# Performance work log

Measured on AMD Instinct MI355X. Metric: run time of the kernel, lower is better.

Reference implementation:

```python
import jax, jax.numpy as jnp
import numpy as np

N = 262144        # 64^3 grid unknowns
NNZ = 7 * N       # ~7-point stencil sparsity
BS = 32


def setup_inputs() -> dict:
    key = jax.random.key(0)
    k1, k2, k3, k4, k5 = jax.random.split(key, 5)
    y_pred = jax.random.normal(k1, (BS, N), dtype=jnp.float32)
    y_true = jax.random.normal(k2, (BS, N), dtype=jnp.float32)
    A_vals = jax.random.normal(k3, (NNZ,), dtype=jnp.float32)
    A_rows = jax.random.randint(k4, (NNZ,), 0, N, dtype=jnp.int32)
    A_cols = jax.random.randint(k5, (NNZ,), 0, N, dtype=jnp.int32)
    return {"y_pred": y_pred, "y_true": y_true, "A_vals": A_vals,
            "A_rows": A_rows, "A_cols": A_cols}


def reference(y_pred, y_true, A_vals, A_rows, A_cols):
    # YhatY[b] = <y_true[b], y_pred[b]>
    YhatY = jnp.sum(y_true * y_pred, axis=1)                      # (bs,)
    # Sparse matvec per batch: YhatAt = (A @ y_pred.T).T, COO form.
    # gathered[e, b] = A_vals[e] * y_pred[b, A_cols[e]]
    gathered = (y_pred[:, A_cols] * A_vals).T                     # (nnz, bs)
    YhatAt = jax.ops.segment_sum(gathered, A_rows, num_segments=N).T  # (bs, N)
    # YhatYhatAt[b] = <y_pred[b], A y_pred[b]>
    YhatYhatAt = jnp.sum(y_pred * YhatAt, axis=1)                 # (bs,)
    # diag(YhatY / YhatYhatAt) @ YhatAt == row-wise scale by alpha
    alpha = YhatY / YhatYhatAt                                    # (bs,)
    resid = y_true - alpha[:, None] * YhatAt                      # (bs, N)
    return jnp.mean(jnp.sum(resid * resid, axis=1))
```

## Files before the change

### kernel.cpp

```cpp
#include <hip/hip_runtime.h>

#define NGRID 262144
#define NNZ_C 1835008
#define TP    260


__global__ __launch_bounds__(256) void k_prep(
        const float* __restrict__ yp, const float* __restrict__ yt,
        float* __restrict__ yp_t, float* __restrict__ yat_t,
        float* __restrict__ p1) {
    __shared__ __align__(16) float T[32 * TP];
    __shared__ float p1red[32];
    const int tid = threadIdx.x;
    const int l = tid & 63, w = tid >> 6;
    const size_t n0 = (size_t)blockIdx.x * 256;
    #pragma unroll
    for (int s = 0; s < 8; ++s) {
        const int b = s * 4 + w;
        const float4 a = *(const float4*)(yp + (size_t)b * NGRID + n0 + 4 * l);
        const float4 t = *(const float4*)(yt + (size_t)b * NGRID + n0 + 4 * l);
        *(float4*)(&T[b * TP + 4 * l]) = a;
        float sty = a.x * t.x + a.y * t.y + a.z * t.z + a.w * t.w;
        #pragma unroll
        for (int o = 32; o > 0; o >>= 1) sty += __shfl_down(sty, o);
        if (l == 0) p1red[b] = sty;
    }
    __syncthreads();
    float4* ypt4 = (float4*)(yp_t + n0 * 32);
    float4* yat4 = (float4*)(yat_t + n0 * 32);
    #pragma unroll
    for (int q = 0; q < 8; ++q) {
        const int f = q * 256 + tid;
        const int n = f >> 3;
        const int bb = 4 * (f & 7);
        float4 v;
        v.x = T[(bb + 0) * TP + n];
        v.y = T[(bb + 1) * TP + n];
        v.z = T[(bb + 2) * TP + n];
        v.w = T[(bb + 3) * TP + n];
        ypt4[f] = v;
        yat4[f] = make_float4(0.f, 0.f, 0.f, 0.f);
    }
    if (tid < 32) p1[blockIdx.x * 32 + tid] = p1red[tid];
}

__global__ void k_scatter(const float* __restrict__ vals,
                          const int* __restrict__ rows,
                          const int* __restrict__ cols,
                          const float* __restrict__ yp_t,
                          float* __restrict__ yat_t) {
    const size_t tid = (size_t)blockIdx.x * blockDim.x + threadIdx.x;
    const int b = (int)(tid & 31);
    const size_t e = tid >> 5;
    const float v = vals[e];
    const int r = rows[e];
    const int c = cols[e];
    const float x = yp_t[(size_t)c * 32 + b];
    atomicAdd(&yat_t[(size_t)r * 32 + b], v * x);
}

__global__ __launch_bounds__(256) void k_post(
        const float* __restrict__ yat_t, const float* __restrict__ yp_t,
        const float* __restrict__ yt, float* __restrict__ p2) {
    __shared__ float tile[256 * 33];
    __shared__ float red[2][256];
    const int tid = threadIdx.x;
    const size_t n0 = (size_t)blockIdx.x * 256;

    float c1 = 0.f, c3 = 0.f;
    #pragma unroll
    for (int i = 0; i < 32; ++i) {
        const int f = i * 256 + tid;
        const float a = yat_t[n0 * 32 + f];
        const float p = yp_t[n0 * 32 + f];
        c1 = fmaf(p, a, c1);
        c3 = fmaf(a, a, c3);
        tile[(f >> 5) * 33 + (f & 31)] = a;
    }
    red[0][tid] = c1;
    red[1][tid] = c3;
    __syncthreads();

    const int w = tid >> 6;
    const int lane = tid & 63;
    #pragma unroll
    for (int j = 0; j < 8; ++j) {
        const int b = w * 8 + j;
        const float* ytr = yt + (size_t)b * NGRID + n0;
        float c2 = 0.f, tt = 0.f;
        #pragma unroll
        for (int c = 0; c < 4; ++c) {
            const int nl = c * 64 + lane;
            const float t = ytr[nl];
            const float yv = tile[nl * 33 + b];
            c2 = fmaf(t, yv, c2);
            tt = fmaf(t, t, tt);
        }
        #pragma unroll
        for (int o = 32; o > 0; o >>= 1) {
            c2 += __shfl_down(c2, o);
            tt += __shfl_down(tt, o);
        }
        if (lane == 0) {
            p2[blockIdx.x * 128 + 32 + b] = c2;
            p2[blockIdx.x * 128 + 96 + b] = tt;
        }
    }

    if (tid < 32) {
        float s1 = 0.f, s3 = 0.f;
        #pragma unroll
        for (int k = 0; k < 8; ++k) {
            s1 += red[0][tid + 32 * k];
            s3 += red[1][tid + 32 * k];
        }
        p2[blockIdx.x * 128 + 0 + tid] = s1;
        p2[blockIdx.x * 128 + 64 + tid] = s3;
    }
}

__global__ __launch_bounds__(256) void k_finish(
        const float* __restrict__ p2, const float* __restrict__ p1,
        float* __restrict__ out) {
    __shared__ float tot[128];
    __shared__ float styv[32];
    __shared__ float lb[32];
    const int tid = threadIdx.x;
    if (tid < 128) {
        float acc = 0.f;
        for (int j = 0; j < 1024; ++j) acc += p2[(size_t)j * 128 + tid];
        tot[tid] = acc;
    } else if (tid < 160) {
        const int b = tid - 128;
        float acc = 0.f;
        for (int j = 0; j < 1024; ++j) acc += p1[(size_t)j * 32 + b];
        styv[b] = acc;
    }
    __syncthreads();
    if (tid < 32) {
        const float c1 = tot[tid];
        const float c2 = tot[32 + tid];
        const float c3 = tot[64 + tid];
        const float stt = tot[96 + tid];
        const float a = styv[tid] / c1;
        lb[tid] = fmaf(a * a, c3, fmaf(-2.f * a, c2, stt));
    }
    __syncthreads();
    if (tid == 0) {
        float s = 0.f;
        #pragma unroll
        for (int i = 0; i < 32; ++i) s += lb[i];
        out[0] = s * (1.0f / 32.0f);
    }
}

extern "C" void kernel_launch(void* const* d_in, const int* in_sizes, int n_in,
                              void* d_out, int out_size, void* d_ws, size_t ws_size,
                              hipStream_t stream) {
    const float* yp = (const float*)d_in[0];
    const float* yt = (const float*)d_in[1];
    const float* Av = (const float*)d_in[2];
    const int*   Ar = (const int*)d_in[3];
    const int*   Ac = (const int*)d_in[4];
    float* out = (float*)d_out;

    float* ws    = (float*)d_ws;
    float* yp_t  = ws;
    float* yat_t = yp_t + (size_t)NGRID * 32;
    float* p1    = yat_t + (size_t)NGRID * 32;
    float* p2    = p1 + 1024 * 32;

    k_prep<<<NGRID / 256, 256, 0, stream>>>(yp, yt, yp_t, yat_t, p1);
    k_scatter<<<(NNZ_C * 32) / 256, 256, 0, stream>>>(Av, Ar, Ac, yp_t, yat_t);
    k_post<<<NGRID / 256, 256, 0, stream>>>(yat_t, yp_t, yt, p2);
    k_finish<<<1, 256, 0, stream>>>(p2, p1, out);
}
```

Measured before the change: 348.1 us.

## Use packed float2 atomics in scatter, vectorize post loads, split final reduction

The scatter kernel now handles two batch columns per thread and issues packed v2f32 atomic adds where the builtin exists, halving the atomic instruction count and thread count. k_post reads y_true with float4 loads and gathers its per-batch sums through shared memory. The single-block final reduction over 1024 partials becomes a two-stage reduction across 64 blocks plus one block. Packed atomics depend on compiler builtin availability, and if neither is present the code falls back to two scalar atomics.

```diff
diff --git a/kernel.cpp b/kernel.cpp
--- a/kernel.cpp
+++ b/kernel.cpp
@@ -4,6 +4,15 @@
 #define NNZ_C 1835008
 #define TP    260
 
+
+typedef float v2f __attribute__((ext_vector_type(2)));
+#ifdef __has_builtin
+#if __has_builtin(__builtin_amdgcn_flat_atomic_fadd_v2f32)
+#define PK_FADD_FLAT 1
+#elif __has_builtin(__builtin_amdgcn_global_atomic_fadd_v2f32)
+#define PK_FADD_GLOBAL 1
+#endif
+#endif
 
 __global__ __launch_bounds__(256) void k_prep(
         const float* __restrict__ yp, const float* __restrict__ yt,
@@ -50,13 +59,24 @@
                           const float* __restrict__ yp_t,
                           float* __restrict__ yat_t) {
     const size_t tid = (size_t)blockIdx.x * blockDim.x + threadIdx.x;
-    const int b = (int)(tid & 31);
-    const size_t e = tid >> 5;
+    const int b2 = (int)(tid & 15);
+    const size_t e = tid >> 4;
     const float v = vals[e];
     const int r = rows[e];
     const int c = cols[e];
-    const float x = yp_t[(size_t)c * 32 + b];
-    atomicAdd(&yat_t[(size_t)r * 32 + b], v * x);
+    const float2 x = *(const float2*)(yp_t + (size_t)c * 32 + 2 * b2);
+    float* dst = yat_t + (size_t)r * 32 + 2 * b2;
+#if defined(PK_FADD_FLAT)
+    v2f add; add.x = v * x.x; add.y = v * x.y;
+    __builtin_amdgcn_flat_atomic_fadd_v2f32((v2f*)dst, add);
+#elif defined(PK_FADD_GLOBAL)
+    v2f add; add.x = v * x.x; add.y = v * x.y;
+    __builtin_amdgcn_global_atomic_fadd_v2f32(
+        (__attribute__((address_space(1))) v2f*)(unsigned long long)dst, add);
+#else
+    atomicAdd(dst, v * x.x);
+    atomicAdd(dst + 1, v * x.y);
+#endif
 }
 
 __global__ __launch_bounds__(256) void k_post(
@@ -64,7 +84,9 @@
         const float* __restrict__ yt, float* __restrict__ p2) {
     __shared__ float tile[256 * 33];
     __shared__ float red[2][256];
+    __shared__ float c2red[32], ttred[32];
     const int tid = threadIdx.x;
+    const int l = tid & 63, w = tid >> 6;
     const size_t n0 = (size_t)blockIdx.x * 256;
 
     float c1 = 0.f, c3 = 0.f;
@@ -81,31 +103,22 @@
     red[1][tid] = c3;
     __syncthreads();
 
-    const int w = tid >> 6;
-    const int lane = tid & 63;
-    #pragma unroll
-    for (int j = 0; j < 8; ++j) {
-        const int b = w * 8 + j;
-        const float* ytr = yt + (size_t)b * NGRID + n0;
-        float c2 = 0.f, tt = 0.f;
-        #pragma unroll
-        for (int c = 0; c < 4; ++c) {
-            const int nl = c * 64 + lane;
-            const float t = ytr[nl];
-            const float yv = tile[nl * 33 + b];
-            c2 = fmaf(t, yv, c2);
-            tt = fmaf(t, t, tt);
-        }
+    #pragma unroll
+    for (int s = 0; s < 8; ++s) {
+        const int b = 4 * s + w;
+        const float4 t = *(const float4*)(yt + (size_t)b * NGRID + n0 + 4 * l);
+        const int n = 4 * l;
+        float c2 = t.x * tile[(n + 0) * 33 + b] + t.y * tile[(n + 1) * 33 + b]
+                 + t.z * tile[(n + 2) * 33 + b] + t.w * tile[(n + 3) * 33 + b];
+        float tt = t.x * t.x + t.y * t.y + t.z * t.z + t.w * t.w;
         #pragma unroll
         for (int o = 32; o > 0; o >>= 1) {
             c2 += __shfl_down(c2, o);
             tt += __shfl_down(tt, o);
         }
-        if (lane == 0) {
-            p2[blockIdx.x * 128 + 32 + b] = c2;
-            p2[blockIdx.x * 128 + 96 + b] = tt;
-        }
-    }
+        if (l == 0) { c2red[b] = c2; ttred[b] = tt; }
+    }
+    __syncthreads();
 
     if (tid < 32) {
         float s1 = 0.f, s3 = 0.f;
@@ -115,12 +128,32 @@
             s3 += red[1][tid + 32 * k];
         }
         p2[blockIdx.x * 128 + 0 + tid] = s1;
+        p2[blockIdx.x * 128 + 32 + tid] = c2red[tid];
         p2[blockIdx.x * 128 + 64 + tid] = s3;
-    }
-}
-
-__global__ __launch_bounds__(256) void k_finish(
+        p2[blockIdx.x * 128 + 96 + tid] = ttred[tid];
+    }
+}
+
+__global__ __launch_bounds__(256) void k_finish1(
         const float* __restrict__ p2, const float* __restrict__ p1,
+        float* __restrict__ pr2, float* __restrict__ pr1) {
+    const int tid = threadIdx.x, g = blockIdx.x;
+    if (tid < 128) {
+        float acc = 0.f;
+        #pragma unroll
+        for (int j = 0; j < 16; ++j) acc += p2[(size_t)(g * 16 + j) * 128 + tid];
+        pr2[g * 128 + tid] = acc;
+    } else if (tid < 160) {
+        const int b = tid - 128;
+        float acc = 0.f;
+        #pragma unroll
+        for (int j = 0; j < 16; ++j) acc += p1[(size_t)(g * 16 + j) * 32 + b];
+        pr1[g * 32 + b] = acc;
+    }
+}
+
+__global__ __launch_bounds__(256) void k_finish2(
+        const float* __restrict__ pr2, const float* __restrict__ pr1,
         float* __restrict__ out) {
     __shared__ float tot[128];
     __shared__ float styv[32];
@@ -128,12 +161,14 @@
     const int tid = threadIdx.x;
     if (tid < 128) {
         float acc = 0.f;
-        for (int j = 0; j < 1024; ++j) acc += p2[(size_t)j * 128 + tid];
+        #pragma unroll
+        for (int j = 0; j < 64; ++j) acc += pr2[j * 128 + tid];
         tot[tid] = acc;
     } else if (tid < 160) {
         const int b = tid - 128;
         float acc = 0.f;
-        for (int j = 0; j < 1024; ++j) acc += p1[(size_t)j * 32 + b];
+        #pragma unroll
+        for (int j = 0; j < 64; ++j) acc += pr1[j * 32 + b];
         styv[b] = acc;
     }
     __syncthreads();
@@ -169,9 +204,12 @@
     float* yat_t = yp_t + (size_t)NGRID * 32;
     float* p1    = yat_t + (size_t)NGRID * 32;
     float* p2    = p1 + 1024 * 32;
+    float* pr1   = p2 + 1024 * 128;
+    float* pr2   = pr1 + 64 * 32;
 
     k_prep<<<NGRID / 256, 256, 0, stream>>>(yp, yt, yp_t, yat_t, p1);
-    k_scatter<<<(NNZ_C * 32) / 256, 256, 0, stream>>>(Av, Ar, Ac, yp_t, yat_t);
+    k_scatter<<<(NNZ_C * 16) / 256, 256, 0, stream>>>(Av, Ar, Ac, yp_t, yat_t);
     k_post<<<NGRID / 256, 256, 0, stream>>>(yat_t, yp_t, yt, p2);
-    k_finish<<<1, 256, 0, stream>>>(p2, p1, out);
-}
+    k_finish1<<<64, 256, 0, stream>>>(p2, p1, pr2, pr1);
+    k_finish2<<<1, 256, 0, stream>>>(pr2, pr1, out);
+}
```

New measurement: 501.7 us. 1.44x slower.
